# Kernel tuning notes

Hardware: AMD Instinct MI355X
Metric: run time of the kernel (lower is better)

Reference implementation:

```python
import jax, jax.numpy as jnp
import numpy as np

B, T, L, V, E, H = 128, 64, 2, 32000, 768, 768
G = 4 * H  # gate dim
EPS = 1e-5


def setup_inputs() -> dict:
    key = jax.random.key(0)
    ks = jax.random.split(key, 12)
    s = 1.0 / np.sqrt(H)
    message = jax.random.randint(ks[0], (B, T), 0, V, dtype=jnp.int64)
    message_lengths = jax.random.randint(ks[1], (B,), 1, T + 1, dtype=jnp.int64)
    return {
        "message": message,
        "message_lengths": message_lengths,
        "embedding_table": jax.random.normal(ks[2], (V, E), jnp.float32),
        "W_ih": jax.random.uniform(ks[3], (L, G, E), jnp.float32, -s, s),
        "W_hh": jax.random.uniform(ks[4], (L, G, H), jnp.float32, -s, s),
        "b_ih": jax.random.uniform(ks[5], (L, G), jnp.float32, -s, s),
        "b_hh": jax.random.uniform(ks[6], (L, G), jnp.float32, -s, s),
        "gamma_h": 1.0 + 0.1 * jax.random.normal(ks[7], (H,), jnp.float32),
        "beta_h": 0.1 * jax.random.normal(ks[8], (H,), jnp.float32),
        "gamma_c": 1.0 + 0.1 * jax.random.normal(ks[9], (H,), jnp.float32),
        "beta_c": 0.1 * jax.random.normal(ks[10], (H,), jnp.float32),
    }


def _layernorm(x, g, b):
    mu = jnp.mean(x, axis=-1, keepdims=True)
    var = jnp.mean(jnp.square(x - mu), axis=-1, keepdims=True)
    return (x - mu) * jax.lax.rsqrt(var + EPS) * g + b


def reference(message, message_lengths, embedding_table, W_ih, W_hh, b_ih, b_hh,
              gamma_h, beta_h, gamma_c, beta_c):
    emb = embedding_table[message]  # [B, T, E]
    # Precompute input projections for all steps/layers (every layer sees the
    # raw embedding at each step, matching the original code).
    x_proj = jnp.einsum('bte,lge->tblg', emb, W_ih) + b_ih  # [T, B, L, G]
    mask = jnp.ones((B, H), emb.dtype)  # dropout_rate=None -> ones mask

    h0 = jnp.zeros((L, B, H), emb.dtype)
    c0 = jnp.zeros((L, B, H), emb.dtype)

    def step(carry, x_t):  # x_t: [B, L, G]
        h, c = carry
        new_h, new_c = [], []
        h_last = None
        for l in range(L):
            gates = x_t[:, l] + h[l] @ W_hh[l].T + b_hh[l]  # [B, G]
            i_g, f_g, g_g, o_g = jnp.split(gates, 4, axis=-1)
            c_t = jax.nn.sigmoid(f_g) * c[l] + jax.nn.sigmoid(i_g) * jnp.tanh(g_g)
            h_t = jax.nn.sigmoid(o_g) * jnp.tanh(c_t)
            h_t = _layernorm(h_t * mask, gamma_h, beta_h)
            c_t = _layernorm(c_t, gamma_c, beta_c)
            new_h.append(h_t)
            new_c.append(c_t)
            h_last = h_t
        return (jnp.stack(new_h), jnp.stack(new_c)), h_last

    _, hidden_all = jax.lax.scan(step, (h0, c0), x_proj)  # [T, B, H]
    hidden_all = hidden_all.transpose(1, 0, 2)  # [B, T, H]
    idx = (message_lengths - 1)[:, None, None]  # [B, 1, 1]
    encoded = jnp.take_along_axis(hidden_all, idx, axis=1)[:, 0]  # [B, H]
    return encoded
```

## Files before the change

### kernel.cpp

```cpp
#include <hip/hip_runtime.h>
#include <stdint.h>

#define T_LEN 64
#define B_SZ  128
#define H_SZ  768
#define G_SZ  3072
#define E_SZ  768
#define LN_EPS 1e-5f

typedef __bf16 bf16x8 __attribute__((ext_vector_type(8)));
typedef float  f32x4  __attribute__((ext_vector_type(4)));
typedef short  short8 __attribute__((ext_vector_type(8)));

__device__ __forceinline__ float bf2f(unsigned short h) {
  unsigned int u = ((unsigned int)h) << 16;
  return __builtin_bit_cast(float, u);
}
__device__ __forceinline__ unsigned short f2bf(float f) {
  unsigned int u = __builtin_bit_cast(unsigned int, f);
  u += 0x7fffu + ((u >> 16) & 1u);
  return (unsigned short)(u >> 16);
}
__device__ __forceinline__ void split8(float4 v0, float4 v1, short8& hi, short8& lo) {
  float v[8] = {v0.x, v0.y, v0.z, v0.w, v1.x, v1.y, v1.z, v1.w};
#pragma unroll
  for (int j = 0; j < 8; ++j) {
    unsigned short h = f2bf(v[j]);
    hi[j] = (short)h;
    lo[j] = (short)f2bf(v[j] - bf2f(h));
  }
}
__device__ __forceinline__ void st_wt(void* p, unsigned long long v) {
  __hip_atomic_store((unsigned long long*)p, v, __ATOMIC_RELAXED,
                     __HIP_MEMORY_SCOPE_AGENT);
}

__global__ void prep_kernel(const int* __restrict__ msg,
                            const float* __restrict__ table,
                            const float* __restrict__ W_ih,
                            const float* __restrict__ W_hh,
                            const float* __restrict__ b_ih,
                            const float* __restrict__ b_hh,
                            const float* __restrict__ gamma_h,
                            const float* __restrict__ beta_h,
                            unsigned short* __restrict__ A_hi,
                            unsigned short* __restrict__ A_lo,
                            unsigned short* __restrict__ Wih_hi,
                            unsigned short* __restrict__ Wih_lo,
                            unsigned short* __restrict__ Whh_hi,
                            unsigned short* __restrict__ Whh_lo,
                            float* __restrict__ SWp,
                            float* __restrict__ Sbeta,
                            float* __restrict__ bias,
                            unsigned int* __restrict__ bar) {
  int idx = blockIdx.x * blockDim.x + threadIdx.x;
  int stride = gridDim.x * blockDim.x;
  for (int c = idx; c < 8192 * 96; c += stride) {
    int n = c / 96;
    int ko = (c - n * 96) * 8;
    int b = n & 127, t = n >> 7;
    int m = msg[b * T_LEN + t];
    const float4* s4 = (const float4*)(table + (size_t)m * E_SZ + ko);
    short8 hi, lo;
    split8(s4[0], s4[1], hi, lo);
    *(short8*)(A_hi + (size_t)n * E_SZ + ko) = hi;
    *(short8*)(A_lo + (size_t)n * E_SZ + ko) = lo;
  }
  for (int c = idx; c < G_SZ * E_SZ / 8; c += stride) {
    int o8 = c * 8;
    {
      const float4* s4 = (const float4*)(W_ih + (size_t)G_SZ * E_SZ + o8);
      short8 hi, lo;
      split8(s4[0], s4[1], hi, lo);
      *(short8*)(Wih_hi + o8) = hi;
      *(short8*)(Wih_lo + o8) = lo;
    }
    {
      int g = o8 / H_SZ;
      int j = o8 - g * H_SZ;
      const float4* s4 = (const float4*)(W_hh + (size_t)G_SZ * H_SZ + o8);
      const float4* g4 = (const float4*)(gamma_h + j);
      float4 v0 = s4[0], v1 = s4[1];
      float4 w0 = g4[0], w1 = g4[1];
      v0.x *= w0.x; v0.y *= w0.y; v0.z *= w0.z; v0.w *= w0.w;
      v1.x *= w1.x; v1.y *= w1.y; v1.z *= w1.z; v1.w *= w1.w;
      short8 hi, lo;
      split8(v0, v1, hi, lo);
      *(short8*)(Whh_hi + o8) = hi;
      *(short8*)(Whh_lo + o8) = lo;
    }
  }
  for (int g = idx; g < G_SZ; g += stride) {
    const float4* wr = (const float4*)(W_hh + (size_t)G_SZ * H_SZ + (size_t)g * H_SZ);
    const float4* gm = (const float4*)gamma_h;
    const float4* bt = (const float4*)beta_h;
    float sw = 0.f, sb = 0.f;
    for (int i = 0; i < H_SZ / 4; ++i) {
      float4 wv = wr[i], gv = gm[i], bv = bt[i];
      sw += wv.x * gv.x + wv.y * gv.y + wv.z * gv.z + wv.w * gv.w;
      sb += wv.x * bv.x + wv.y * bv.y + wv.z * bv.z + wv.w * bv.w;
    }
    SWp[g] = sw;
    Sbeta[g] = sb;
    bias[g] = b_ih[G_SZ + g] + b_hh[G_SZ + g];
  }
  for (int c = idx; c < 18432; c += stride) bar[c] = 0u;
}

#define K2_STR 56

__global__ __launch_bounds__(256) void xproj_kernel(
    const unsigned short* __restrict__ A_hi, const unsigned short* __restrict__ A_lo,
    const unsigned short* __restrict__ B_hi, const unsigned short* __restrict__ B_lo,
    const float* __restrict__ bias, void* __restrict__ Xout, int x_is_f32) {
  __shared__ float smemf[7168];
  unsigned short* AsH = (unsigned short*)smemf;
  unsigned short* AsL = AsH + 64 * K2_STR;
  unsigned short* BsH = AsL + 64 * K2_STR;
  unsigned short* BsL = BsH + 64 * K2_STR;

  int bid = blockIdx.x;
  int mchunk = bid / 384;
  int r = bid - mchunk * 384;
  int nb = r >> 3;
  int mb = (mchunk << 3) + (r & 7);
  int m0 = mb * 64, n0 = nb * 64;
  int tid = threadIdx.x;
  int w = tid >> 6, lane = tid & 63;
  int wm = w & 1, wn = w >> 1;
  int rs = tid >> 2, ks = (tid & 3) * 8;
  int lrow = lane & 15, lk = (lane >> 4) * 8;

  f32x4 acc[2][2] = {};
  const unsigned short* gA = A_hi + (size_t)(m0 + rs) * E_SZ + ks;
  const unsigned short* gAl = A_lo + (size_t)(m0 + rs) * E_SZ + ks;
  const unsigned short* gB = B_hi + (size_t)(n0 + rs) * E_SZ + ks;
  const unsigned short* gBl = B_lo + (size_t)(n0 + rs) * E_SZ + ks;
  short8 vah = *(const short8*)gA;
  short8 val = *(const short8*)gAl;
  short8 vbh = *(const short8*)gB;
  short8 vbl = *(const short8*)gBl;
  for (int kt = 0; kt < 24; ++kt) {
    __syncthreads();
    *(short8*)(AsH + rs * K2_STR + ks) = vah;
    *(short8*)(AsL + rs * K2_STR + ks) = val;
    *(short8*)(BsH + rs * K2_STR + ks) = vbh;
    *(short8*)(BsL + rs * K2_STR + ks) = vbl;
    __syncthreads();
    if (kt < 23) {
      int k0 = (kt + 1) * 32;
      vah = *(const short8*)(gA + k0);
      val = *(const short8*)(gAl + k0);
      vbh = *(const short8*)(gB + k0);
      vbl = *(const short8*)(gBl + k0);
    }
    bf16x8 ah0 = *(const bf16x8*)(AsH + (wm * 32 +      lrow) * K2_STR + lk);
    bf16x8 ah1 = *(const bf16x8*)(AsH + (wm * 32 + 16 + lrow) * K2_STR + lk);
    bf16x8 al0 = *(const bf16x8*)(AsL + (wm * 32 +      lrow) * K2_STR + lk);
    bf16x8 al1 = *(const bf16x8*)(AsL + (wm * 32 + 16 + lrow) * K2_STR + lk);
    bf16x8 bh0 = *(const bf16x8*)(BsH + (wn * 32 +      lrow) * K2_STR + lk);
    bf16x8 bh1 = *(const bf16x8*)(BsH + (wn * 32 + 16 + lrow) * K2_STR + lk);
    bf16x8 bl0 = *(const bf16x8*)(BsL + (wn * 32 +      lrow) * K2_STR + lk);
    bf16x8 bl1 = *(const bf16x8*)(BsL + (wn * 32 + 16 + lrow) * K2_STR + lk);
    acc[0][0] = __builtin_amdgcn_mfma_f32_16x16x32_bf16(ah0, bh0, acc[0][0], 0, 0, 0);
    acc[1][0] = __builtin_amdgcn_mfma_f32_16x16x32_bf16(ah1, bh0, acc[1][0], 0, 0, 0);
    acc[0][1] = __builtin_amdgcn_mfma_f32_16x16x32_bf16(ah0, bh1, acc[0][1], 0, 0, 0);
    acc[1][1] = __builtin_amdgcn_mfma_f32_16x16x32_bf16(ah1, bh1, acc[1][1], 0, 0, 0);
    acc[0][0] = __builtin_amdgcn_mfma_f32_16x16x32_bf16(al0, bh0, acc[0][0], 0, 0, 0);
    acc[1][0] = __builtin_amdgcn_mfma_f32_16x16x32_bf16(al1, bh0, acc[1][0], 0, 0, 0);
    acc[0][1] = __builtin_amdgcn_mfma_f32_16x16x32_bf16(al0, bh1, acc[0][1], 0, 0, 0);
    acc[1][1] = __builtin_amdgcn_mfma_f32_16x16x32_bf16(al1, bh1, acc[1][1], 0, 0, 0);
    acc[0][0] = __builtin_amdgcn_mfma_f32_16x16x32_bf16(ah0, bl0, acc[0][0], 0, 0, 0);
    acc[1][0] = __builtin_amdgcn_mfma_f32_16x16x32_bf16(ah1, bl0, acc[1][0], 0, 0, 0);
    acc[0][1] = __builtin_amdgcn_mfma_f32_16x16x32_bf16(ah0, bl1, acc[0][1], 0, 0, 0);
    acc[1][1] = __builtin_amdgcn_mfma_f32_16x16x32_bf16(ah1, bl1, acc[1][1], 0, 0, 0);
  }
  __syncthreads();
  float* Cs = smemf;
  int quad = lane >> 4;
#pragma unroll
  for (int mt = 0; mt < 2; ++mt)
#pragma unroll
    for (int nt = 0; nt < 2; ++nt) {
      int mloc = wm * 32 + mt * 16 + quad * 4;
      int nloc = wn * 32 + nt * 16 + lrow;
#pragma unroll
      for (int rr = 0; rr < 4; ++rr) Cs[nloc * 72 + mloc + rr] = acc[mt][nt][rr];
    }
  __syncthreads();
  int t = mb >> 1, bbase = (mb & 1) * 64;
#pragma unroll
  for (int rep = 0; rep < 2; ++rep) {
    int n = (tid >> 3) + rep * 32;
    int c = (tid & 7) * 8;
    float bv = bias[n0 + n];
    float v[8];
#pragma unroll
    for (int j = 0; j < 8; ++j) v[j] = Cs[n * 72 + c + j] + bv;
    size_t off = ((size_t)t * G_SZ + (n0 + n)) * B_SZ + bbase + c;
    if (x_is_f32) {
      float4* dst = (float4*)((float*)Xout + off);
      dst[0] = make_float4(v[0], v[1], v[2], v[3]);
      dst[1] = make_float4(v[4], v[5], v[6], v[7]);
    } else {
      short8 o;
#pragma unroll
      for (int j = 0; j < 8; ++j) o[j] = (short)f2bf(v[j]);
      *(short8*)((unsigned short*)Xout + off) = o;
    }
  }
}

__device__ __forceinline__ void gridbar(unsigned int* leaf, unsigned int* root,
                                        int idx, int sub) {
  __syncthreads();
  if (threadIdx.x == 0) {
    asm volatile("" ::: "memory");
    unsigned int old = __hip_atomic_fetch_add(&leaf[idx * 128 + sub * 16], 1u,
                                              __ATOMIC_RELAXED, __HIP_MEMORY_SCOPE_AGENT);
    if (old == 11u)
      __hip_atomic_fetch_add(&root[idx * 16], 1u,
                             __ATOMIC_RELAXED, __HIP_MEMORY_SCOPE_AGENT);
    while (__hip_atomic_load(&root[idx * 16], __ATOMIC_RELAXED,
                             __HIP_MEMORY_SCOPE_AGENT) < 8u)
      __builtin_amdgcn_s_sleep(2);
    asm volatile("" ::: "memory");
  }
  __syncthreads();
}

extern __shared__ char lstm_smem[];

__global__ __launch_bounds__(128) void lstm_kernel(
    const unsigned short* __restrict__ Whh_lo,
    const unsigned short* __restrict__ Whh_hi,
    const void* __restrict__ X, int x_is_f32,
    const float* __restrict__ SWp, const float* __restrict__ Sbeta,
    const float* __restrict__ gamma_h, const float* __restrict__ beta_h,
    const float* __restrict__ gamma_c, const float* __restrict__ beta_c,
    const int* __restrict__ lens,
    unsigned short* __restrict__ Hbuf, float* __restrict__ part,
    unsigned int* __restrict__ bar, float* __restrict__ out) {
  unsigned short* WtH = (unsigned short*)lstm_smem;
  unsigned short* WtL = WtH + 32 * 776;
  float* glds   = (float*)(WtL + 32 * 776);
  float* pstat2 = glds + 2304;
  float* rstat4 = pstat2 + 512;
  float* rstat  = rstat4 + 256;
  float* ghs = rstat + 256;
  float* bhs = ghs + 8;
  float* gcs = bhs + 8;
  float* bcs = gcs + 8;

  int bidx = blockIdx.x;
  int jb = bidx % 96, rb = bidx / 96;
  int j0 = jb * 8, b0 = rb * 64;
  int tid = threadIdx.x;
  int w = tid >> 6, lane = tid & 63;
  int lrow = lane & 15, lkq = lane >> 4;
  int sub = jb / 12;
  unsigned int* leaf = bar;
  unsigned int* root = bar + 16384;

  for (int c = tid; c < 3072; c += 128) {
    int row = c / 96, ko = (c - row * 96) * 8;
    size_t goff = ((size_t)((row >> 3) * H_SZ + j0 + (row & 7))) * H_SZ + ko;
    *(short8*)(&WtH[row * 776 + ko]) = *(const short8*)(Whh_hi + goff);
    *(short8*)(&WtL[row * 776 + ko]) = *(const short8*)(Whh_lo + goff);
  }
  if (tid < 8) {
    ghs[tid] = gamma_h[j0 + tid]; bhs[tid] = beta_h[j0 + tid];
    gcs[tid] = gamma_c[j0 + tid]; bcs[tid] = beta_c[j0 + tid];
  }

  int row = tid & 63;
  int half = tid >> 6;
  int jjq = half * 4;
  int mylen = lens[b0 + row];
  int myWrow = (w << 4) | lrow;
  int gate4 = myWrow >> 3, jjl = myWrow & 7;
  int g_global = gate4 * H_SZ + j0 + jjl;
  float mySW = SWp[g_global];
  float mySb = Sbeta[g_global];
  const unsigned short* wbase = &WtH[(size_t)myWrow * 776];
  const unsigned short* wlob  = &WtL[(size_t)myWrow * 776];
  float c4[4], h4[4];
  float xv[4][4];
  __syncthreads();

  {
    size_t xbase = ((size_t)0 * G_SZ + g_global) * B_SZ + b0 + lkq * 4;
#pragma unroll
    for (int mt = 0; mt < 4; ++mt) {
      float xr[4];
      if (x_is_f32) {
        float4 p = *(const float4*)((const float*)X + xbase + mt * 16);
        xr[0] = p.x; xr[1] = p.y; xr[2] = p.z; xr[3] = p.w;
      } else {
        ushort4 p = *(const ushort4*)((const unsigned short*)X + xbase + mt * 16);
        xr[0] = bf2f(p.x); xr[1] = bf2f(p.y); xr[2] = bf2f(p.z); xr[3] = bf2f(p.w);
      }
#pragma unroll
      for (int rr = 0; rr < 4; ++rr)
        glds[(gate4 * 8 + jjl) * 72 + mt * 16 + lkq * 4 + rr] = xr[rr];
    }
  }
  __syncthreads();
  {
    float ph = 0.f, ph2 = 0.f, pc = 0.f, pc2 = 0.f;
#pragma unroll
    for (int q = 0; q < 4; ++q) {
      int jj = jjq + q;
      float iv = glds[(0 * 8 + jj) * 72 + row];
      float gv = glds[(2 * 8 + jj) * 72 + row];
      float ov = glds[(3 * 8 + jj) * 72 + row];
      float si = 1.f / (1.f + expf(-iv));
      float so = 1.f / (1.f + expf(-ov));
      float cn = si * tanhf(gv);
      float hp = so * tanhf(cn);
      c4[q] = cn; h4[q] = hp;
      ph += hp; ph2 += hp * hp; pc += cn; pc2 += cn * cn;
    }
    size_t hx = (((size_t)0 * 128 + b0 + row) * 96 + jb) * 32 + jjq;
    ushort4 hiv, lov;
    hiv.x = f2bf(h4[0]); hiv.y = f2bf(h4[1]); hiv.z = f2bf(h4[2]); hiv.w = f2bf(h4[3]);
    lov.x = f2bf(h4[0] - bf2f(hiv.x)); lov.y = f2bf(h4[1] - bf2f(hiv.y));
    lov.z = f2bf(h4[2] - bf2f(hiv.z)); lov.w = f2bf(h4[3] - bf2f(hiv.w));
    st_wt(&Hbuf[hx], __builtin_bit_cast(unsigned long long, hiv));
    st_wt(&Hbuf[hx + 8], __builtin_bit_cast(unsigned long long, lov));
    *(f32x4*)&pstat2[(row * 2 + half) * 4] = f32x4{ph, ph2, pc, pc2};
  }
  __syncthreads();
  {
    int f = tid * 2;
    float2 v;
    v.x = pstat2[(f >> 2) * 8 + (f & 3)] + pstat2[(f >> 2) * 8 + 4 + (f & 3)];
    v.y = pstat2[((f + 1) >> 2) * 8 + ((f + 1) & 3)] +
          pstat2[((f + 1) >> 2) * 8 + 4 + ((f + 1) & 3)];
    st_wt(&part[((size_t)(0 * 2 + rb) * 96 + jb) * 256 + f],
          __builtin_bit_cast(unsigned long long, v));
  }
  {
    size_t xbase = ((size_t)1 * G_SZ + g_global) * B_SZ + b0 + lkq * 4;
#pragma unroll
    for (int mt = 0; mt < 4; ++mt) {
      if (x_is_f32) {
        float4 p = *(const float4*)((const float*)X + xbase + mt * 16);
        xv[mt][0] = p.x; xv[mt][1] = p.y; xv[mt][2] = p.z; xv[mt][3] = p.w;
      } else {
        ushort4 p = *(const ushort4*)((const unsigned short*)X + xbase + mt * 16);
        xv[mt][0] = bf2f(p.x); xv[mt][1] = bf2f(p.y);
        xv[mt][2] = bf2f(p.z); xv[mt][3] = bf2f(p.w);
      }
    }
  }
  gridbar(leaf, root, 0 * 2 + rb, sub);

  for (int t = 1; t < T_LEN; ++t) {
    f32x4 acc[4] = {};
    {
      const unsigned short* hb[4];
#pragma unroll
      for (int mt = 0; mt < 4; ++mt)
        hb[mt] = Hbuf + ((size_t)(t - 1) * 128 + b0 + mt * 16 + lrow) * 3072;
#pragma unroll 4
      for (int kt = 0; kt < 24; ++kt) {
        int k0 = kt * 32 + lkq * 8;
        int co = (kt * 4 + lkq) * 32;
        bf16x8 wh = *(const bf16x8*)(wbase + k0);
        bf16x8 wl = *(const bf16x8*)(wlob + k0);
#pragma unroll
        for (int mt = 0; mt < 4; ++mt) {
          bf16x8 ah = *(const bf16x8*)(hb[mt] + co);
          bf16x8 al = *(const bf16x8*)(hb[mt] + co + 8);
          acc[mt] = __builtin_amdgcn_mfma_f32_16x16x32_bf16(ah, wh, acc[mt], 0, 0, 0);
          acc[mt] = __builtin_amdgcn_mfma_f32_16x16x32_bf16(al, wh, acc[mt], 0, 0, 0);
          acc[mt] = __builtin_amdgcn_mfma_f32_16x16x32_bf16(ah, wl, acc[mt], 0, 0, 0);
        }
      }
    }
    float psum0 = 0.f, psum1 = 0.f;
    {
      const float* pb = part + ((size_t)((t - 1) * 2 + rb) * 96) * 256 + tid * 2;
#pragma unroll 8
      for (int j = 0; j < 96; ++j) {
        float2 v = *(const float2*)(pb + j * 256);
        psum0 += v.x; psum1 += v.y;
      }
    }
    {
      int f = tid * 2;
      rstat4[f] = psum0;
      rstat4[f + 1] = psum1;
    }
    __syncthreads();
    if (tid < 64) {
      f32x4 s = *(f32x4*)&rstat4[tid * 4];
      float muh = s[0] * (1.f / 768.f), muc = s[2] * (1.f / 768.f);
      float vh = s[1] * (1.f / 768.f) - muh * muh;
      float vc = s[3] * (1.f / 768.f) - muc * muc;
      float rh = rsqrtf(vh + LN_EPS), rc = rsqrtf(vc + LN_EPS);
      *(f32x4*)&rstat[tid * 4] = f32x4{rh, muh * rh, rc, muc * rc};
    }
    __syncthreads();
    {
      int told = t - 1;
      if (told == mylen - 1) {
        float2 rv = *(float2*)&rstat[row * 4];
#pragma unroll
        for (int q = 0; q < 4; ++q)
          out[(size_t)(b0 + row) * H_SZ + j0 + jjq + q] =
              (rv.x * h4[q] - rv.y) * ghs[jjq + q] + bhs[jjq + q];
      }
    }
    __syncthreads();
#pragma unroll
    for (int mt = 0; mt < 4; ++mt) {
#pragma unroll
      for (int rr = 0; rr < 4; ++rr) {
        int r2 = mt * 16 + lkq * 4 + rr;
        float2 rv = *(float2*)&rstat[r2 * 4];
        glds[(gate4 * 8 + jjl) * 72 + r2] =
            xv[mt][rr] + rv.x * acc[mt][rr] - rv.y * mySW + mySb;
      }
    }
    __syncthreads();
    {
      f32x4 rv = *(f32x4*)&rstat[row * 4];
      float ph = 0.f, ph2 = 0.f, pc = 0.f, pc2 = 0.f;
#pragma unroll
      for (int q = 0; q < 4; ++q) {
        int jj = jjq + q;
        float cprev = (rv[2] * c4[q] - rv[3]) * gcs[jj] + bcs[jj];
        float iv = glds[(0 * 8 + jj) * 72 + row];
        float fv = glds[(1 * 8 + jj) * 72 + row];
        float gv = glds[(2 * 8 + jj) * 72 + row];
        float ov = glds[(3 * 8 + jj) * 72 + row];
        float si = 1.f / (1.f + expf(-iv));
        float sf = 1.f / (1.f + expf(-fv));
        float so = 1.f / (1.f + expf(-ov));
        float cn = sf * cprev + si * tanhf(gv);
        float hp = so * tanhf(cn);
        c4[q] = cn; h4[q] = hp;
        ph += hp; ph2 += hp * hp; pc += cn; pc2 += cn * cn;
      }
      size_t hx = (((size_t)t * 128 + b0 + row) * 96 + jb) * 32 + jjq;
      ushort4 hiv, lov;
      hiv.x = f2bf(h4[0]); hiv.y = f2bf(h4[1]); hiv.z = f2bf(h4[2]); hiv.w = f2bf(h4[3]);
      lov.x = f2bf(h4[0] - bf2f(hiv.x)); lov.y = f2bf(h4[1] - bf2f(hiv.y));
      lov.z = f2bf(h4[2] - bf2f(hiv.z)); lov.w = f2bf(h4[3] - bf2f(hiv.w));
      st_wt(&Hbuf[hx], __builtin_bit_cast(unsigned long long, hiv));
      st_wt(&Hbuf[hx + 8], __builtin_bit_cast(unsigned long long, lov));
      *(f32x4*)&pstat2[(row * 2 + half) * 4] = f32x4{ph, ph2, pc, pc2};
    }
    __syncthreads();
    {
      int f = tid * 2;
      float2 v;
      v.x = pstat2[(f >> 2) * 8 + (f & 3)] + pstat2[(f >> 2) * 8 + 4 + (f & 3)];
      v.y = pstat2[((f + 1) >> 2) * 8 + ((f + 1) & 3)] +
            pstat2[((f + 1) >> 2) * 8 + 4 + ((f + 1) & 3)];
      st_wt(&part[((size_t)(t * 2 + rb) * 96 + jb) * 256 + f],
            __builtin_bit_cast(unsigned long long, v));
    }
    if (t < T_LEN - 1) {
      size_t xbase = ((size_t)(t + 1) * G_SZ + g_global) * B_SZ + b0 + lkq * 4;
#pragma unroll
      for (int mt = 0; mt < 4; ++mt) {
        if (x_is_f32) {
          float4 p = *(const float4*)((const float*)X + xbase + mt * 16);
          xv[mt][0] = p.x; xv[mt][1] = p.y; xv[mt][2] = p.z; xv[mt][3] = p.w;
        } else {
          ushort4 p = *(const ushort4*)((const unsigned short*)X + xbase + mt * 16);
          xv[mt][0] = bf2f(p.x); xv[mt][1] = bf2f(p.y);
          xv[mt][2] = bf2f(p.z); xv[mt][3] = bf2f(p.w);
        }
      }
    }
    gridbar(leaf, root, t * 2 + rb, sub);
  }

  {
    float psum0 = 0.f, psum1 = 0.f;
    const float* pb = part + ((size_t)(63 * 2 + rb) * 96) * 256 + tid * 2;
#pragma unroll 8
    for (int j = 0; j < 96; ++j) {
      float2 v = *(const float2*)(pb + j * 256);
      psum0 += v.x; psum1 += v.y;
    }
    rstat4[tid * 2] = psum0;
    rstat4[tid * 2 + 1] = psum1;
  }
  __syncthreads();
  if (tid < 64) {
    f32x4 s = *(f32x4*)&rstat4[tid * 4];
    float muh = s[0] * (1.f / 768.f);
    float vh = s[1] * (1.f / 768.f) - muh * muh;
    float rh = rsqrtf(vh + LN_EPS);
    rstat[tid * 4] = rh;
    rstat[tid * 4 + 1] = muh * rh;
  }
  __syncthreads();
  if (mylen == T_LEN) {
    float2 rv = *(float2*)&rstat[row * 4];
#pragma unroll
    for (int q = 0; q < 4; ++q)
      out[(size_t)(b0 + row) * H_SZ + j0 + jjq + q] =
          (rv.x * h4[q] - rv.y) * ghs[jjq + q] + bhs[jjq + q];
  }
}

#define LSTM_LDS_BYTES 112896

extern "C" void kernel_launch(void* const* d_in, const int* in_sizes, int n_in,
                              void* d_out, int out_size, void* d_ws, size_t ws_size,
                              hipStream_t stream) {
  const int*   msg     = (const int*)d_in[0];
  const int*   lens    = (const int*)d_in[1];
  const float* table   = (const float*)d_in[2];
  const float* W_ih    = (const float*)d_in[3];
  const float* W_hh    = (const float*)d_in[4];
  const float* b_ih    = (const float*)d_in[5];
  const float* b_hh    = (const float*)d_in[6];
  const float* gamma_h = (const float*)d_in[7];
  const float* beta_h  = (const float*)d_in[8];
  const float* gamma_c = (const float*)d_in[9];
  const float* beta_c  = (const float*)d_in[10];
  float* out = (float*)d_out;

  static int attr_done = 0;
  if (!attr_done) {
    hipFuncSetAttribute((const void*)lstm_kernel,
                        hipFuncAttributeMaxDynamicSharedMemorySize,
                        LSTM_LDS_BYTES);
    attr_done = 1;
  }

  size_t szA = (size_t)8192 * 768 * 2;
  size_t szW = (size_t)3072 * 768 * 2;
  size_t szF = 3072 * 4;
  size_t szH = (size_t)T_LEN * 128 * 96 * 32 * 2;
  size_t szBar = 18432 * 4;
  size_t rest = 2 * szA + 4 * szW + 3 * szF + szH + szBar;
  size_t xf32 = (size_t)64 * 3072 * 128 * 4;
  int x_is_f32 = (ws_size >= xf32 + rest) ? 1 : 0;

  char* p = (char*)d_ws;
  void* X = (void*)p;               p += x_is_f32 ? xf32 : (xf32 / 2);
  unsigned short* A_hi   = (unsigned short*)p; p += szA;
  unsigned short* A_lo   = (unsigned short*)p; p += szA;
  unsigned short* Wih_hi = (unsigned short*)p; p += szW;
  unsigned short* Wih_lo = (unsigned short*)p; p += szW;
  unsigned short* Whh_hi = (unsigned short*)p; p += szW;
  unsigned short* Whh_lo = (unsigned short*)p; p += szW;
  float* SWp   = (float*)p;         p += szF;
  float* Sbeta = (float*)p;         p += szF;
  float* bias  = (float*)p;         p += szF;
  unsigned short* Hbuf = (unsigned short*)p; p += szH;
  unsigned int* bar = (unsigned int*)p;      p += szBar;
  float* part = (float*)A_hi;

  hipLaunchKernelGGL(prep_kernel, dim3(1024), dim3(256), 0, stream,
                     msg, table, W_ih, W_hh, b_ih, b_hh, gamma_h, beta_h,
                     A_hi, A_lo, Wih_hi, Wih_lo, Whh_hi, Whh_lo,
                     SWp, Sbeta, bias, bar);
  hipLaunchKernelGGL(xproj_kernel, dim3(6144), dim3(256), 0, stream,
                     A_hi, A_lo, Wih_hi, Wih_lo, bias, X, x_is_f32);

  void* kargs[] = { (void*)&Whh_lo, (void*)&Whh_hi, (void*)&X, (void*)&x_is_f32,
                    (void*)&SWp, (void*)&Sbeta,
                    (void*)&gamma_h, (void*)&beta_h, (void*)&gamma_c, (void*)&beta_c,
                    (void*)&lens, (void*)&Hbuf, (void*)&part,
                    (void*)&bar, (void*)&out };
  hipLaunchCooperativeKernel((void*)lstm_kernel, dim3(192), dim3(128), kargs,
                             LSTM_LDS_BYTES, stream);
}
```

Measured before the change: 1.855 ms.

## Reduce LayerNorm partial stats with global atomics and compact hidden-state buffer

Each block now atomically adds its per-row LayerNorm partial sums into a single per-step accumulator in global memory, which prep_kernel zeroes beforehand. Previously it wrote 96 separate partials that every block then re-read and summed after the grid barrier. This drops a 96-iteration global read loop and a block sync from each timestep, so the post-barrier work is two loads per thread. The hidden-state buffer row stride is also halved from 32 to 16 elements, removing padding and shrinking the footprint of the matmul loads. The cost is contended float atomics on the same addresses from many blocks and a summation order that is no longer deterministic.

```diff
diff --git a/kernel.cpp b/kernel.cpp
--- a/kernel.cpp
+++ b/kernel.cpp
@@ -33,6 +33,13 @@
 __device__ __forceinline__ void st_wt(void* p, unsigned long long v) {
   __hip_atomic_store((unsigned long long*)p, v, __ATOMIC_RELAXED,
                      __HIP_MEMORY_SCOPE_AGENT);
+}
+__device__ __forceinline__ unsigned long long ld_cp(const void* p) {
+  return __hip_atomic_load((const unsigned long long*)p, __ATOMIC_RELAXED,
+                           __HIP_MEMORY_SCOPE_AGENT);
+}
+__device__ __forceinline__ void at_add(float* p, float v) {
+  __hip_atomic_fetch_add(p, v, __ATOMIC_RELAXED, __HIP_MEMORY_SCOPE_AGENT);
 }
 
 __global__ void prep_kernel(const int* __restrict__ msg,
@@ -52,7 +59,8 @@
                             float* __restrict__ SWp,
                             float* __restrict__ Sbeta,
                             float* __restrict__ bias,
-                            unsigned int* __restrict__ bar) {
+                            unsigned int* __restrict__ bar,
+                            float* __restrict__ part) {
   int idx = blockIdx.x * blockDim.x + threadIdx.x;
   int stride = gridDim.x * blockDim.x;
   for (int c = idx; c < 8192 * 96; c += stride) {
@@ -105,6 +113,8 @@
     bias[g] = b_ih[G_SZ + g] + b_hh[G_SZ + g];
   }
   for (int c = idx; c < 18432; c += stride) bar[c] = 0u;
+  for (int c = idx; c < 128 * 256 / 2; c += stride)
+    st_wt((unsigned long long*)part + c, 0ull);
 }
 
 #define K2_STR 56
@@ -321,7 +331,7 @@
       c4[q] = cn; h4[q] = hp;
       ph += hp; ph2 += hp * hp; pc += cn; pc2 += cn * cn;
     }
-    size_t hx = (((size_t)0 * 128 + b0 + row) * 96 + jb) * 32 + jjq;
+    size_t hx = (((size_t)0 * 128 + b0 + row) * 96 + jb) * 16 + jjq;
     ushort4 hiv, lov;
     hiv.x = f2bf(h4[0]); hiv.y = f2bf(h4[1]); hiv.z = f2bf(h4[2]); hiv.w = f2bf(h4[3]);
     lov.x = f2bf(h4[0] - bf2f(hiv.x)); lov.y = f2bf(h4[1] - bf2f(hiv.y));
@@ -333,12 +343,12 @@
   __syncthreads();
   {
     int f = tid * 2;
-    float2 v;
-    v.x = pstat2[(f >> 2) * 8 + (f & 3)] + pstat2[(f >> 2) * 8 + 4 + (f & 3)];
-    v.y = pstat2[((f + 1) >> 2) * 8 + ((f + 1) & 3)] +
-          pstat2[((f + 1) >> 2) * 8 + 4 + ((f + 1) & 3)];
-    st_wt(&part[((size_t)(0 * 2 + rb) * 96 + jb) * 256 + f],
-          __builtin_bit_cast(unsigned long long, v));
+    float v0 = pstat2[(f >> 2) * 8 + (f & 3)] + pstat2[(f >> 2) * 8 + 4 + (f & 3)];
+    float v1 = pstat2[((f + 1) >> 2) * 8 + ((f + 1) & 3)] +
+               pstat2[((f + 1) >> 2) * 8 + 4 + ((f + 1) & 3)];
+    float* pp = part + (size_t)(0 * 2 + rb) * 256 + f;
+    at_add(pp, v0);
+    at_add(pp + 1, v1);
   }
   {
     size_t xbase = ((size_t)1 * G_SZ + g_global) * B_SZ + b0 + lkq * 4;
@@ -357,16 +367,25 @@
   gridbar(leaf, root, 0 * 2 + rb, sub);
 
   for (int t = 1; t < T_LEN; ++t) {
+    f32x4 sstat = {};
+    if (tid < 64) {
+      const float* pp = part + (size_t)((t - 1) * 2 + rb) * 256 + tid * 4;
+      unsigned long long a = ld_cp(pp);
+      unsigned long long b = ld_cp(pp + 2);
+      float2 fa = __builtin_bit_cast(float2, a);
+      float2 fb = __builtin_bit_cast(float2, b);
+      sstat = f32x4{fa.x, fa.y, fb.x, fb.y};
+    }
     f32x4 acc[4] = {};
     {
       const unsigned short* hb[4];
 #pragma unroll
       for (int mt = 0; mt < 4; ++mt)
-        hb[mt] = Hbuf + ((size_t)(t - 1) * 128 + b0 + mt * 16 + lrow) * 3072;
+        hb[mt] = Hbuf + ((size_t)(t - 1) * 128 + b0 + mt * 16 + lrow) * 1536;
 #pragma unroll 4
       for (int kt = 0; kt < 24; ++kt) {
         int k0 = kt * 32 + lkq * 8;
-        int co = (kt * 4 + lkq) * 32;
+        int co = (kt * 4 + lkq) * 16;
         bf16x8 wh = *(const bf16x8*)(wbase + k0);
         bf16x8 wl = *(const bf16x8*)(wlob + k0);
 #pragma unroll
@@ -379,41 +398,21 @@
         }
       }
     }
-    float psum0 = 0.f, psum1 = 0.f;
-    {
-      const float* pb = part + ((size_t)((t - 1) * 2 + rb) * 96) * 256 + tid * 2;
-#pragma unroll 8
-      for (int j = 0; j < 96; ++j) {
-        float2 v = *(const float2*)(pb + j * 256);
-        psum0 += v.x; psum1 += v.y;
-      }
-    }
-    {
-      int f = tid * 2;
-      rstat4[f] = psum0;
-      rstat4[f + 1] = psum1;
-    }
-    __syncthreads();
     if (tid < 64) {
-      f32x4 s = *(f32x4*)&rstat4[tid * 4];
-      float muh = s[0] * (1.f / 768.f), muc = s[2] * (1.f / 768.f);
-      float vh = s[1] * (1.f / 768.f) - muh * muh;
-      float vc = s[3] * (1.f / 768.f) - muc * muc;
+      float muh = sstat[0] * (1.f / 768.f), muc = sstat[2] * (1.f / 768.f);
+      float vh = sstat[1] * (1.f / 768.f) - muh * muh;
+      float vc = sstat[3] * (1.f / 768.f) - muc * muc;
       float rh = rsqrtf(vh + LN_EPS), rc = rsqrtf(vc + LN_EPS);
       *(f32x4*)&rstat[tid * 4] = f32x4{rh, muh * rh, rc, muc * rc};
     }
     __syncthreads();
-    {
-      int told = t - 1;
-      if (told == mylen - 1) {
-        float2 rv = *(float2*)&rstat[row * 4];
-#pragma unroll
-        for (int q = 0; q < 4; ++q)
-          out[(size_t)(b0 + row) * H_SZ + j0 + jjq + q] =
-              (rv.x * h4[q] - rv.y) * ghs[jjq + q] + bhs[jjq + q];
-      }
-    }
-    __syncthreads();
+    if (mylen == t) {
+      float2 rv = *(float2*)&rstat[row * 4];
+#pragma unroll
+      for (int q = 0; q < 4; ++q)
+        out[(size_t)(b0 + row) * H_SZ + j0 + jjq + q] =
+            (rv.x * h4[q] - rv.y) * ghs[jjq + q] + bhs[jjq + q];
+    }
 #pragma unroll
     for (int mt = 0; mt < 4; ++mt) {
 #pragma unroll
@@ -444,7 +443,7 @@
         c4[q] = cn; h4[q] = hp;
         ph += hp; ph2 += hp * hp; pc += cn; pc2 += cn * cn;
       }
-      size_t hx = (((size_t)t * 128 + b0 + row) * 96 + jb) * 32 + jjq;
+      size_t hx = (((size_t)t * 128 + b0 + row) * 96 + jb) * 16 + jjq;
       ushort4 hiv, lov;
       hiv.x = f2bf(h4[0]); hiv.y = f2bf(h4[1]); hiv.z = f2bf(h4[2]); hiv.w = f2bf(h4[3]);
       lov.x = f2bf(h4[0] - bf2f(hiv.x)); lov.y = f2bf(h4[1] - bf2f(hiv.y));
@@ -456,12 +455,12 @@
     __syncthreads();
     {
       int f = tid * 2;
-      float2 v;
-      v.x = pstat2[(f >> 2) * 8 + (f & 3)] + pstat2[(f >> 2) * 8 + 4 + (f & 3)];
-      v.y = pstat2[((f + 1) >> 2) * 8 + ((f + 1) & 3)] +
-            pstat2[((f + 1) >> 2) * 8 + 4 + ((f + 1) & 3)];
-      st_wt(&part[((size_t)(t * 2 + rb) * 96 + jb) * 256 + f],
-            __builtin_bit_cast(unsigned long long, v));
+      float v0 = pstat2[(f >> 2) * 8 + (f & 3)] + pstat2[(f >> 2) * 8 + 4 + (f & 3)];
+      float v1 = pstat2[((f + 1) >> 2) * 8 + ((f + 1) & 3)] +
+                 pstat2[((f + 1) >> 2) * 8 + 4 + ((f + 1) & 3)];
+      float* pp = part + (size_t)(t * 2 + rb) * 256 + f;
+      at_add(pp, v0);
+      at_add(pp + 1, v1);
     }
     if (t < T_LEN - 1) {
       size_t xbase = ((size_t)(t + 1) * G_SZ + g_global) * B_SZ + b0 + lkq * 4;
@@ -480,25 +479,18 @@
     gridbar(leaf, root, t * 2 + rb, sub);
   }
 
-  {
-    float psum0 = 0.f, psum1 = 0.f;
-    const float* pb = part + ((size_t)(63 * 2 + rb) * 96) * 256 + tid * 2;
-#pragma unroll 8
-    for (int j = 0; j < 96; ++j) {
-      float2 v = *(const float2*)(pb + j * 256);
-      psum0 += v.x; psum1 += v.y;
-    }
-    rstat4[tid * 2] = psum0;
-    rstat4[tid * 2 + 1] = psum1;
-  }
-  __syncthreads();
   if (tid < 64) {
-    f32x4 s = *(f32x4*)&rstat4[tid * 4];
-    float muh = s[0] * (1.f / 768.f);
-    float vh = s[1] * (1.f / 768.f) - muh * muh;
+    const float* pp = part + (size_t)(63 * 2 + rb) * 256 + tid * 4;
+    unsigned long long a = ld_cp(pp);
+    unsigned long long b = ld_cp(pp + 2);
+    float2 fa = __builtin_bit_cast(float2, a);
+    float2 fb = __builtin_bit_cast(float2, b);
+    float muh = fa.x * (1.f / 768.f);
+    float vh = fa.y * (1.f / 768.f) - muh * muh;
     float rh = rsqrtf(vh + LN_EPS);
     rstat[tid * 4] = rh;
     rstat[tid * 4 + 1] = muh * rh;
+    (void)fb;
   }
   __syncthreads();
   if (mylen == T_LEN) {
@@ -539,9 +531,10 @@
   size_t szA = (size_t)8192 * 768 * 2;
   size_t szW = (size_t)3072 * 768 * 2;
   size_t szF = 3072 * 4;
-  size_t szH = (size_t)T_LEN * 128 * 96 * 32 * 2;
+  size_t szH = (size_t)T_LEN * 128 * 96 * 16 * 2;
   size_t szBar = 18432 * 4;
-  size_t rest = 2 * szA + 4 * szW + 3 * szF + szH + szBar;
+  size_t szPart = (size_t)128 * 256 * 4;
+  size_t rest = 2 * szA + 4 * szW + 3 * szF + szH + szBar + szPart;
   size_t xf32 = (size_t)64 * 3072 * 128 * 4;
   int x_is_f32 = (ws_size >= xf32 + rest) ? 1 : 0;
 
@@ -558,12 +551,12 @@
   float* bias  = (float*)p;         p += szF;
   unsigned short* Hbuf = (unsigned short*)p; p += szH;
   unsigned int* bar = (unsigned int*)p;      p += szBar;
-  float* part = (float*)A_hi;
+  float* part = (float*)p;                   p += szPart;
 
   hipLaunchKernelGGL(prep_kernel, dim3(1024), dim3(256), 0, stream,
                      msg, table, W_ih, W_hh, b_ih, b_hh, gamma_h, beta_h,
                      A_hi, A_lo, Wih_hi, Wih_lo, Whh_hi, Whh_lo,
-                     SWp, Sbeta, bias, bar);
+                     SWp, Sbeta, bias, bar, part);
   hipLaunchKernelGGL(xproj_kernel, dim3(6144), dim3(256), 0, stream,
                      A_hi, A_lo, Wih_hi, Wih_lo, bias, X, x_is_f32);
 
```

New measurement: 3.028 ms. 63.2% more time.
